# Kernel optimization log

Hardware: AMD Instinct MI355X
Metric: run time of the kernel (lower is better)

The kernel has to match this reference:

```python
import jax, jax.numpy as jnp
import numpy as np

N, B, G, D = 262144, 4096, 8, 7
NODE_DIM, GLOBAL_DIM, HIDDEN = 128, 128, 64
NEG = -1000000000.0


def setup_inputs() -> dict:
    key = jax.random.key(0)
    ks = jax.random.split(key, 7)
    node_features = jax.random.normal(ks[0], (N, NODE_DIM), jnp.float32)
    global_features = jax.random.normal(ks[1], (B, GLOBAL_DIM), jnp.float32)
    group_mask_nodes = jax.random.randint(ks[2], (N,), 0, 2) == 1
    batch = jnp.sort(jax.random.randint(ks[3], (N,), 0, B)).astype(jnp.int32)
    maneuver_mask = jax.random.randint(ks[4], (B, G, D), 0, 2) == 1
    W1 = jax.random.normal(ks[5], (NODE_DIM + GLOBAL_DIM, HIDDEN), jnp.float32) * 0.0625
    b1 = jnp.zeros((HIDDEN,), jnp.float32)
    W2 = jax.random.normal(ks[6], (HIDDEN, D), jnp.float32) * 0.125
    b2 = jnp.zeros((D,), jnp.float32)
    return {"node_features": node_features, "global_features": global_features,
            "group_mask_nodes": group_mask_nodes, "batch": batch,
            "maneuver_mask": maneuver_mask, "W1": W1, "b1": b1, "W2": W2, "b2": b2}


def reference(node_features, global_features, group_mask_nodes, batch, maneuver_mask, W1, b1, W2, b2):
    # Per-batch ragged group index: g_idx[i] = (# selected rows with same batch id before i).
    sel = group_mask_nodes
    sel_i = sel.astype(jnp.int32)
    csum = jnp.cumsum(sel_i)                                   # inclusive cumsum over selected rows
    counts = jax.ops.segment_sum(sel_i, batch, num_segments=B)  # selected rows per batch
    offsets = jnp.concatenate([jnp.zeros(1, jnp.int32), jnp.cumsum(counts)[:-1].astype(jnp.int32)])
    g_idx = csum - 1 - offsets[batch]                          # valid only where sel
    valid = sel & (g_idx < G)

    # Batched tiny MLP: concat(node, global[batch]) @ W1 done as split matmul to avoid materializing concat.
    glob = global_features[batch]                              # [N, GLOBAL_DIM] gather
    h = jax.nn.relu(node_features @ W1[:NODE_DIM] + glob @ W1[NODE_DIM:] + b1)
    out = h @ W2 + b2                                          # [N, D]

    # Scatter into padded [B, G+1, D]; invalid rows routed to dummy group slot G (sliced off).
    logits = jnp.full((B, G + 1, D), NEG, dtype=out.dtype)
    b_s = jnp.where(valid, batch, 0)
    g_s = jnp.where(valid, g_idx, G)
    logits = logits.at[b_s, g_s].set(out)
    logits = logits[:, :G, :]
    logits = jnp.where(maneuver_mask, logits, jnp.float32(NEG))
    return logits.reshape(B, G * D)
```

## Files before the change

### kernel.cpp

```cpp
#include <hip/hip_runtime.h>
#include <hip/hip_bf16.h>

#define G_SLOTS   8
#define D_OUT     7
#define NODE_DIM  128
#define GLOB_DIM  128
#define HIDDEN    64
#define NEG_VAL   (-1000000000.0f)
#define XSTRIDE   129
#define GH_STRIDE 68

__global__ void seg_starts_kernel(const int* __restrict__ batch,
                                  int* __restrict__ starts, int N, int B) {
    int i = blockIdx.x * blockDim.x + threadIdx.x;
    if (i >= N) return;
    int b = batch[i];
    if (i == 0) {
        for (int bb = 0; bb <= b; ++bb) starts[bb] = 0;
    } else {
        int pb = batch[i - 1];
        for (int bb = pb + 1; bb <= b; ++bb) starts[bb] = i;
    }
    if (i == N - 1) {
        for (int bb = b + 1; bb <= B; ++bb) starts[bb] = N;
    }
}

__global__ __launch_bounds__(256) void fused_mlp_kernel(
        const float* __restrict__ node,
        const float* __restrict__ glob,
        const int* __restrict__ sel,
        const int* __restrict__ starts,
        const int* __restrict__ mmask,
        const float* __restrict__ W1,
        const float* __restrict__ b1,
        const float* __restrict__ W2,
        const float* __restrict__ b2,
        float* __restrict__ out) {
    __shared__ __align__(16) float w1n[NODE_DIM * HIDDEN];
    __shared__ __align__(16) float xlds[64 * XSTRIDE];
    __shared__ __align__(16) float gh_l[G_SLOTS * GH_STRIDE];
    __shared__ __align__(16) float w2l[HIDDEN * D_OUT];
    __shared__ __align__(16) float b2l[D_OUT + 1];
    __shared__ __align__(16) int   starts_l[G_SLOTS + 1];
    __shared__ __align__(16) int   nidxl[64];

    int t = threadIdx.x;
    int b0 = (int)blockIdx.x * 8;
    int slot0 = (int)blockIdx.x * 64;

#pragma unroll
    for (int it = 0; it < 8; ++it) {
        int idx = it * 256 + t;
        *(float4*)&w1n[idx * 4] = *(const float4*)&W1[idx * 4];
    }
    if (t < 112) *(float4*)&w2l[t * 4] = *(const float4*)&W2[t * 4];
    if (t < D_OUT) b2l[t] = b2[t];
    if (t < 9) starts_l[t] = starts[b0 + t];

    {
        int bb = t >> 5;
        int h0 = (t & 31) * 2;
        const float* grow = glob + (size_t)(b0 + bb) * GLOB_DIM;
        float ax = b1[h0], ay = b1[h0 + 1];
#pragma unroll 8
        for (int k = 0; k < GLOB_DIM; ++k) {
            float g = grow[k];
            ax = fmaf(g, W1[(NODE_DIM + k) * HIDDEN + h0],     ax);
            ay = fmaf(g, W1[(NODE_DIM + k) * HIDDEN + h0 + 1], ay);
        }
        gh_l[bb * GH_STRIDE + h0]     = ax;
        gh_l[bb * GH_STRIDE + h0 + 1] = ay;
    }
    __syncthreads();

    {
        int w = t >> 6, lane = t & 63;
        for (int bi = w * 2; bi < w * 2 + 2; ++bi) {
            int start = starts_l[bi], end = starts_l[bi + 1];
            int found = 0;
            for (int base = start; base < end && found < G_SLOTS; base += 64) {
                int i = base + lane;
                bool s = (i < end) && (sel[i] != 0);
                unsigned long long m = __ballot(s);
                if (s) {
                    int rank = found + __popcll(m & ((1ull << lane) - 1ull));
                    if (rank < G_SLOTS) nidxl[bi * G_SLOTS + rank] = i;
                }
                found += __popcll(m);
            }
            int f = found < G_SLOTS ? found : G_SLOTS;
            if (lane < G_SLOTS - f) nidxl[bi * G_SLOTS + f + lane] = -1;
        }
    }
    __syncthreads();

    {
        int r = t >> 2, q = t & 3;
        int nidx = nidxl[r];
        int cbase = q * 32;
        if (nidx >= 0) {
            const float* src = node + (size_t)nidx * NODE_DIM + cbase;
#pragma unroll
            for (int j = 0; j < 8; ++j) {
                float4 v = *(const float4*)&src[j * 4];
                xlds[r * XSTRIDE + cbase + j * 4 + 0] = v.x;
                xlds[r * XSTRIDE + cbase + j * 4 + 1] = v.y;
                xlds[r * XSTRIDE + cbase + j * 4 + 2] = v.z;
                xlds[r * XSTRIDE + cbase + j * 4 + 3] = v.w;
            }
        } else {
#pragma unroll
            for (int j = 0; j < 32; ++j) xlds[r * XSTRIDE + cbase + j] = 0.0f;
        }
    }
    __syncthreads();

    {
        int sl = t >> 2, part = t & 3;
        int bl = sl >> 3;
        int hbase = part * 16;

        float acc[16];
#pragma unroll
        for (int j = 0; j < 16; ++j) acc[j] = gh_l[bl * GH_STRIDE + hbase + j];

#pragma unroll 4
        for (int k = 0; k < NODE_DIM; ++k) {
            float xk = xlds[sl * XSTRIDE + k];
            float4 w0  = *(const float4*)&w1n[k * HIDDEN + hbase + 0];
            float4 w1v = *(const float4*)&w1n[k * HIDDEN + hbase + 4];
            float4 w2v = *(const float4*)&w1n[k * HIDDEN + hbase + 8];
            float4 w3v = *(const float4*)&w1n[k * HIDDEN + hbase + 12];
            acc[0]  = fmaf(xk, w0.x,  acc[0]);  acc[1]  = fmaf(xk, w0.y,  acc[1]);
            acc[2]  = fmaf(xk, w0.z,  acc[2]);  acc[3]  = fmaf(xk, w0.w,  acc[3]);
            acc[4]  = fmaf(xk, w1v.x, acc[4]);  acc[5]  = fmaf(xk, w1v.y, acc[5]);
            acc[6]  = fmaf(xk, w1v.z, acc[6]);  acc[7]  = fmaf(xk, w1v.w, acc[7]);
            acc[8]  = fmaf(xk, w2v.x, acc[8]);  acc[9]  = fmaf(xk, w2v.y, acc[9]);
            acc[10] = fmaf(xk, w2v.z, acc[10]); acc[11] = fmaf(xk, w2v.w, acc[11]);
            acc[12] = fmaf(xk, w3v.x, acc[12]); acc[13] = fmaf(xk, w3v.y, acc[13]);
            acc[14] = fmaf(xk, w3v.z, acc[14]); acc[15] = fmaf(xk, w3v.w, acc[15]);
        }

        float p[D_OUT];
#pragma unroll
        for (int d = 0; d < D_OUT; ++d) p[d] = (part == 0) ? b2l[d] : 0.0f;
#pragma unroll
        for (int hh = 0; hh < 16; ++hh) {
            float h = fmaxf(acc[hh], 0.0f);
            const float* w2row = &w2l[(hbase + hh) * D_OUT];
#pragma unroll
            for (int d = 0; d < D_OUT; ++d) p[d] = fmaf(h, w2row[d], p[d]);
        }
#pragma unroll
        for (int d = 0; d < D_OUT; ++d) {
            p[d] += __shfl_xor(p[d], 1);
            p[d] += __shfl_xor(p[d], 2);
        }
        if (part == 0) {
            int nidx = nidxl[sl];
            int obase = (slot0 + sl) * D_OUT;
#pragma unroll
            for (int d = 0; d < D_OUT; ++d) {
                bool mk = mmask[obase + d] != 0;
                out[obase + d] = (nidx >= 0 && mk) ? p[d] : NEG_VAL;
            }
        }
    }
}

extern "C" void kernel_launch(void* const* d_in, const int* in_sizes, int n_in,
                              void* d_out, int out_size, void* d_ws, size_t ws_size,
                              hipStream_t stream) {
    const float* node  = (const float*)d_in[0];
    const float* glob  = (const float*)d_in[1];
    const int*   sel   = (const int*)d_in[2];
    const int*   batch = (const int*)d_in[3];
    const int*   mmask = (const int*)d_in[4];
    const float* W1    = (const float*)d_in[5];
    const float* b1    = (const float*)d_in[6];
    const float* W2    = (const float*)d_in[7];
    const float* b2    = (const float*)d_in[8];
    float* out = (float*)d_out;

    int N = in_sizes[3];
    int B = in_sizes[1] / GLOB_DIM;

    int* starts = (int*)d_ws;

    seg_starts_kernel<<<(N + 255) / 256, 256, 0, stream>>>(batch, starts, N, B);
    fused_mlp_kernel<<<(B * G_SLOTS) / 64, 256, 0, stream>>>(
        node, glob, sel, starts, mmask, W1, b1, W2, b2, out);
}
```

Before: 204.8 us.

## Compute first MLP layer with fp16 MFMA over concatenated node and global inputs

Replaces the scalar fp32 FMA first layer with MFMA 16x16x32 fp16 matrix instructions. Node rows and the per-batch global features are packed into one fp16 tile, so the 256-wide K covers both halves of W1 and the separate global projection is dropped. W1 is transposed to fp16 in shared memory, and the second layer is split across waves with a partial-sum reduction through LDS. fp16 inputs reduce precision, the global projection is now recomputed per slot instead of per batch, and W1 is converted from global memory on every block.

```diff
diff --git a/kernel.cpp b/kernel.cpp
--- a/kernel.cpp
+++ b/kernel.cpp
@@ -7,8 +7,12 @@
 #define GLOB_DIM  128
 #define HIDDEN    64
 #define NEG_VAL   (-1000000000.0f)
-#define XSTRIDE   129
-#define GH_STRIDE 68
+#define ROW_H     272
+#define H_STRIDE  68
+#define POUT_OFF  4352
+
+typedef _Float16 half8 __attribute__((ext_vector_type(8)));
+typedef float    f32x4 __attribute__((ext_vector_type(4)));
 
 __global__ void seg_starts_kernel(const int* __restrict__ batch,
                                   int* __restrict__ starts, int N, int B) {
@@ -37,40 +41,44 @@
         const float* __restrict__ W2,
         const float* __restrict__ b2,
         float* __restrict__ out) {
-    __shared__ __align__(16) float w1n[NODE_DIM * HIDDEN];
-    __shared__ __align__(16) float xlds[64 * XSTRIDE];
-    __shared__ __align__(16) float gh_l[G_SLOTS * GH_STRIDE];
-    __shared__ __align__(16) float w2l[HIDDEN * D_OUT];
-    __shared__ __align__(16) float b2l[D_OUT + 1];
-    __shared__ __align__(16) int   starts_l[G_SLOTS + 1];
-    __shared__ __align__(16) int   nidxl[64];
+    __shared__ __align__(16) _Float16 xa[64 * ROW_H];
+    __shared__ __align__(16) _Float16 wt[64 * ROW_H];
+    __shared__ __align__(16) int starts_l[G_SLOTS + 1];
+    __shared__ __align__(16) int nidxl[64];
 
     int t = threadIdx.x;
     int b0 = (int)blockIdx.x * 8;
     int slot0 = (int)blockIdx.x * 64;
 
-#pragma unroll
-    for (int it = 0; it < 8; ++it) {
-        int idx = it * 256 + t;
-        *(float4*)&w1n[idx * 4] = *(const float4*)&W1[idx * 4];
-    }
-    if (t < 112) *(float4*)&w2l[t * 4] = *(const float4*)&W2[t * 4];
-    if (t < D_OUT) b2l[t] = b2[t];
     if (t < 9) starts_l[t] = starts[b0 + t];
 
     {
-        int bb = t >> 5;
-        int h0 = (t & 31) * 2;
-        const float* grow = glob + (size_t)(b0 + bb) * GLOB_DIM;
-        float ax = b1[h0], ay = b1[h0 + 1];
-#pragma unroll 8
-        for (int k = 0; k < GLOB_DIM; ++k) {
-            float g = grow[k];
-            ax = fmaf(g, W1[(NODE_DIM + k) * HIDDEN + h0],     ax);
-            ay = fmaf(g, W1[(NODE_DIM + k) * HIDDEN + h0 + 1], ay);
-        }
-        gh_l[bb * GH_STRIDE + h0]     = ax;
-        gh_l[bb * GH_STRIDE + h0 + 1] = ay;
+        int n = t & 63, ko8 = (t >> 6) * 8;
+#pragma unroll
+        for (int it = 0; it < 8; ++it) {
+            int k0 = it * 32 + ko8;
+            half8 hv;
+#pragma unroll
+            for (int j = 0; j < 8; ++j) {
+                hv[j] = (_Float16)W1[(k0 + j) * HIDDEN + n];
+            }
+            *(half8*)&wt[n * ROW_H + k0] = hv;
+        }
+    }
+
+    {
+        int r = t >> 2, q = t & 3;
+        const float* gsrc = glob + (size_t)(b0 + (r >> 3)) * GLOB_DIM + q * 32;
+        int dst = r * ROW_H + 128 + q * 32;
+#pragma unroll
+        for (int jj = 0; jj < 4; ++jj) {
+            half8 hv;
+#pragma unroll
+            for (int j = 0; j < 8; ++j) {
+                hv[j] = (_Float16)gsrc[jj * 8 + j];
+            }
+            *(half8*)&xa[dst + jj * 8] = hv;
+        }
     }
     __syncthreads();
 
@@ -98,73 +106,99 @@
     {
         int r = t >> 2, q = t & 3;
         int nidx = nidxl[r];
-        int cbase = q * 32;
+        int dst = r * ROW_H + q * 32;
         if (nidx >= 0) {
-            const float* src = node + (size_t)nidx * NODE_DIM + cbase;
-#pragma unroll
-            for (int j = 0; j < 8; ++j) {
-                float4 v = *(const float4*)&src[j * 4];
-                xlds[r * XSTRIDE + cbase + j * 4 + 0] = v.x;
-                xlds[r * XSTRIDE + cbase + j * 4 + 1] = v.y;
-                xlds[r * XSTRIDE + cbase + j * 4 + 2] = v.z;
-                xlds[r * XSTRIDE + cbase + j * 4 + 3] = v.w;
+            const float* src = node + (size_t)nidx * NODE_DIM + q * 32;
+#pragma unroll
+            for (int jj = 0; jj < 4; ++jj) {
+                half8 hv;
+#pragma unroll
+                for (int j = 0; j < 8; ++j) {
+                    hv[j] = (_Float16)src[jj * 8 + j];
+                }
+                *(half8*)&xa[dst + jj * 8] = hv;
             }
         } else {
-#pragma unroll
-            for (int j = 0; j < 32; ++j) xlds[r * XSTRIDE + cbase + j] = 0.0f;
-        }
-    }
-    __syncthreads();
-
-    {
-        int sl = t >> 2, part = t & 3;
-        int bl = sl >> 3;
-        int hbase = part * 16;
-
-        float acc[16];
-#pragma unroll
-        for (int j = 0; j < 16; ++j) acc[j] = gh_l[bl * GH_STRIDE + hbase + j];
-
-#pragma unroll 4
-        for (int k = 0; k < NODE_DIM; ++k) {
-            float xk = xlds[sl * XSTRIDE + k];
-            float4 w0  = *(const float4*)&w1n[k * HIDDEN + hbase + 0];
-            float4 w1v = *(const float4*)&w1n[k * HIDDEN + hbase + 4];
-            float4 w2v = *(const float4*)&w1n[k * HIDDEN + hbase + 8];
-            float4 w3v = *(const float4*)&w1n[k * HIDDEN + hbase + 12];
-            acc[0]  = fmaf(xk, w0.x,  acc[0]);  acc[1]  = fmaf(xk, w0.y,  acc[1]);
-            acc[2]  = fmaf(xk, w0.z,  acc[2]);  acc[3]  = fmaf(xk, w0.w,  acc[3]);
-            acc[4]  = fmaf(xk, w1v.x, acc[4]);  acc[5]  = fmaf(xk, w1v.y, acc[5]);
-            acc[6]  = fmaf(xk, w1v.z, acc[6]);  acc[7]  = fmaf(xk, w1v.w, acc[7]);
-            acc[8]  = fmaf(xk, w2v.x, acc[8]);  acc[9]  = fmaf(xk, w2v.y, acc[9]);
-            acc[10] = fmaf(xk, w2v.z, acc[10]); acc[11] = fmaf(xk, w2v.w, acc[11]);
-            acc[12] = fmaf(xk, w3v.x, acc[12]); acc[13] = fmaf(xk, w3v.y, acc[13]);
-            acc[14] = fmaf(xk, w3v.z, acc[14]); acc[15] = fmaf(xk, w3v.w, acc[15]);
-        }
-
+            half8 hz;
+#pragma unroll
+            for (int j = 0; j < 8; ++j) hz[j] = (_Float16)0.0f;
+#pragma unroll
+            for (int jj = 0; jj < 4; ++jj) *(half8*)&xa[dst + jj * 8] = hz;
+        }
+    }
+    __syncthreads();
+
+    int w = t >> 6, lane = t & 63;
+    int col = lane & 15, quad = lane >> 4;
+    f32x4 acc0, acc1, acc2, acc3;
+    acc0 = 0.0f; acc1 = 0.0f; acc2 = 0.0f; acc3 = 0.0f;
+    {
+        int nrow = w * 16 + col;
+#pragma unroll
+        for (int kt = 0; kt < 8; ++kt) {
+            half8 bf = *(const half8*)&wt[nrow * ROW_H + kt * 32 + quad * 8];
+            half8 a0 = *(const half8*)&xa[(0 * 16 + col) * ROW_H + kt * 32 + quad * 8];
+            half8 a1 = *(const half8*)&xa[(1 * 16 + col) * ROW_H + kt * 32 + quad * 8];
+            half8 a2 = *(const half8*)&xa[(2 * 16 + col) * ROW_H + kt * 32 + quad * 8];
+            half8 a3 = *(const half8*)&xa[(3 * 16 + col) * ROW_H + kt * 32 + quad * 8];
+            acc0 = __builtin_amdgcn_mfma_f32_16x16x32_f16(a0, bf, acc0, 0, 0, 0);
+            acc1 = __builtin_amdgcn_mfma_f32_16x16x32_f16(a1, bf, acc1, 0, 0, 0);
+            acc2 = __builtin_amdgcn_mfma_f32_16x16x32_f16(a2, bf, acc2, 0, 0, 0);
+            acc3 = __builtin_amdgcn_mfma_f32_16x16x32_f16(a3, bf, acc3, 0, 0, 0);
+        }
+    }
+    int nh = w * 16 + col;
+    float b1v = b1[nh];
+    __syncthreads();
+
+    {
+        float* H = (float*)wt;
+#pragma unroll
+        for (int reg = 0; reg < 4; ++reg) {
+            int m0 = quad * 4 + reg;
+            H[(m0 +  0) * H_STRIDE + nh] = fmaxf(acc0[reg] + b1v, 0.0f);
+            H[(m0 + 16) * H_STRIDE + nh] = fmaxf(acc1[reg] + b1v, 0.0f);
+            H[(m0 + 32) * H_STRIDE + nh] = fmaxf(acc2[reg] + b1v, 0.0f);
+            H[(m0 + 48) * H_STRIDE + nh] = fmaxf(acc3[reg] + b1v, 0.0f);
+        }
+    }
+    __syncthreads();
+
+    {
+        const float* H = (const float*)wt;
+        float* pout = (float*)wt + POUT_OFF;
+        int sl = t & 63;
+        int partu = t >> 6;
         float p[D_OUT];
 #pragma unroll
-        for (int d = 0; d < D_OUT; ++d) p[d] = (part == 0) ? b2l[d] : 0.0f;
-#pragma unroll
-        for (int hh = 0; hh < 16; ++hh) {
-            float h = fmaxf(acc[hh], 0.0f);
-            const float* w2row = &w2l[(hbase + hh) * D_OUT];
-#pragma unroll
-            for (int d = 0; d < D_OUT; ++d) p[d] = fmaf(h, w2row[d], p[d]);
-        }
-#pragma unroll
-        for (int d = 0; d < D_OUT; ++d) {
-            p[d] += __shfl_xor(p[d], 1);
-            p[d] += __shfl_xor(p[d], 2);
-        }
-        if (part == 0) {
-            int nidx = nidxl[sl];
-            int obase = (slot0 + sl) * D_OUT;
+        for (int d = 0; d < D_OUT; ++d) p[d] = 0.0f;
+#pragma unroll
+        for (int jj = 0; jj < 4; ++jj) {
+            float4 hq = *(const float4*)&H[sl * H_STRIDE + partu * 16 + jj * 4];
+            float hv0 = hq.x, hv1 = hq.y, hv2 = hq.z, hv3 = hq.w;
+            int n0 = partu * 16 + jj * 4;
 #pragma unroll
             for (int d = 0; d < D_OUT; ++d) {
-                bool mk = mmask[obase + d] != 0;
-                out[obase + d] = (nidx >= 0 && mk) ? p[d] : NEG_VAL;
-            }
+                float s = fmaf(hv0, W2[(n0 + 0) * D_OUT + d], p[d]);
+                s = fmaf(hv1, W2[(n0 + 1) * D_OUT + d], s);
+                s = fmaf(hv2, W2[(n0 + 2) * D_OUT + d], s);
+                s = fmaf(hv3, W2[(n0 + 3) * D_OUT + d], s);
+                p[d] = s;
+            }
+        }
+#pragma unroll
+        for (int d = 0; d < D_OUT; ++d) pout[partu * 448 + sl * D_OUT + d] = p[d];
+    }
+    __syncthreads();
+
+    {
+        const float* pout = (const float*)wt + POUT_OFF;
+        for (int e = t; e < 64 * D_OUT; e += 256) {
+            int sl = e / D_OUT, d = e - sl * D_OUT;
+            float v = pout[e] + pout[448 + e] + pout[896 + e] + pout[1344 + e] + b2[d];
+            int oidx = slot0 * D_OUT + e;
+            bool ok = (nidxl[sl] >= 0) && (mmask[oidx] != 0);
+            out[oidx] = ok ? v : NEG_VAL;
         }
     }
 }
```

Measured after the change: 190.6 us. 1.07x faster.
